# Optimization experiments

Hardware: AMD Instinct MI355X
Metric: run time of the kernel (lower is better)

## Reference

```python
import jax, jax.numpy as jnp
import numpy as np

TOPK = 0.1   # effective steady-state topk (target_topk)
TAU = 0.0    # topk_tau default: pure sparse output


def setup_inputs() -> dict:
    key = jax.random.key(0)
    x = jax.random.normal(key, (64, 256, 64, 64), dtype=jnp.float32)
    return {"x": x}


def reference(x):
    # sparse_hw: keep top-k |value| positions over the H*W axis per (n, c) row.
    n, c, h, w = x.shape
    hw = h * w
    k = int(max(1, TOPK * hw))  # 409 for 64x64 at topk=0.1
    xr = x.reshape(n, c, hw)
    # torch.topk(x_reshape.abs(), k, dim=2) -> indices of k largest magnitudes
    _, idx = jax.lax.top_k(jnp.abs(xr), k)  # idx: [n, c, k]
    # mask = zeros.scatter_(2, idx, 1)
    mask = jnp.zeros_like(xr).at[
        jnp.arange(n)[:, None, None],
        jnp.arange(c)[None, :, None],
        idx,
    ].set(1.0)
    sparse_x = (mask * xr).reshape(n, c, h, w)
    if TAU == 0.0:
        return sparse_x
    # tau blend: tau * x + (1 - tau) * sparse_x
    return TAU * x + (1.0 - TAU) * sparse_x
```

## Files before the change

kernel.cpp:

```cpp
#include <hip/hip_runtime.h>

#define HW_ 4096
#define KSEL 409
#define NCAND 256
#define LISTCAP 512

template <int N>
__device__ __forceinline__ void scan_find(const unsigned* hist, unsigned kneed,
                                          unsigned* s_bin, unsigned* s_rem, int t) {
  constexpr int C = N >> 6;
  if (t < 64) {
    const int base = N - (t + 1) * C;
    const uint4* hp = (const uint4*)(hist + base);
    unsigned sum = 0;
    #pragma unroll
    for (int j = 0; j < C / 4; ++j) {
      uint4 u = hp[j];
      sum += u.x + u.y + u.z + u.w;
    }
    unsigned inc = sum;
    #pragma unroll
    for (int off = 1; off < 64; off <<= 1) {
      unsigned u = __shfl_up(inc, off);
      if (t >= off) inc += u;
    }
    unsigned long long mb = __ballot(inc >= kneed);
    int cl = __ffsll((unsigned long long)mb) - 1;
    unsigned cumAbove = __shfl(inc, cl) - __shfl(sum, cl);
    int cbase = N - (cl + 1) * C;
    unsigned hval = (t < C) ? hist[cbase + (C - 1 - t)] : 0u;
    unsigned inc2 = hval;
    #pragma unroll
    for (int off = 1; off < 64; off <<= 1) {
      unsigned u = __shfl_up(inc2, off);
      if (t >= off) inc2 += u;
    }
    unsigned long long mb2 = __ballot(cumAbove + inc2 >= kneed);
    int cl2 = __ffsll((unsigned long long)mb2) - 1;
    if (t == cl2) {
      *s_bin = (unsigned)(cbase + (C - 1 - t));
      *s_rem = kneed - (cumAbove + inc2 - hval);
    }
  }
}

extern "C" __global__ void __launch_bounds__(256, 4)
topk_kern(const float* __restrict__ x, float* __restrict__ out) {
  __shared__ __align__(16) unsigned hist[2048];
  __shared__ unsigned sb[3];
  __shared__ unsigned cnt;
  __shared__ unsigned clist[LISTCAP];
  const int t = threadIdx.x;
  const size_t rowoff = (size_t)blockIdx.x * HW_;
  const float4* xr = (const float4*)(x + rowoff);
  float4* orow = (float4*)(out + rowoff);

  float4 v[4];
  unsigned ab[16];
  #pragma unroll
  for (int j = 0; j < 4; ++j) {
    v[j] = xr[t + j * 256];
    ab[4 * j + 0] = __float_as_uint(v[j].x) & 0x7FFFFFFFu;
    ab[4 * j + 1] = __float_as_uint(v[j].y) & 0x7FFFFFFFu;
    ab[4 * j + 2] = __float_as_uint(v[j].z) & 0x7FFFFFFFu;
    ab[4 * j + 3] = __float_as_uint(v[j].w) & 0x7FFFFFFFu;
  }

  const uint4 z4 = make_uint4(0u, 0u, 0u, 0u);
  ((uint4*)hist)[t] = z4;
  ((uint4*)hist)[t + 256] = z4;
  if (t == 0) cnt = 0;
  __syncthreads();
  #pragma unroll
  for (int i = 0; i < 16; ++i) atomicAdd(&hist[ab[i] >> 20], 1u);
  __syncthreads();
  scan_find<2048>(hist, KSEL, &sb[0], &sb[1], t);
  __syncthreads();
  const unsigned b1 = sb[0];
  const unsigned k2 = sb[1];

  #pragma unroll
  for (int i = 0; i < 16; ++i) {
    if ((ab[i] >> 20) == b1) {
      unsigned id = atomicAdd(&cnt, 1u);
      if (id < LISTCAP) clist[id] = ab[i];
    }
  }
  __syncthreads();
  const unsigned m = cnt;

  unsigned T, rem, ceq;
  if (m <= NCAND) {
    if (t < 64) {
      unsigned rq[4];
      bool vq[4];
      #pragma unroll
      for (int q = 0; q < 4; ++q) {
        unsigned idx = (unsigned)t + 64u * q;
        vq[q] = idx < m;
        rq[q] = vq[q] ? (clist[idx] & 0xFFFFFu) : 0u;
      }
      unsigned p = 0, need = k2;
      #pragma unroll
      for (int b = 19; b >= 0; --b) {
        unsigned trial = p | (1u << b);
        unsigned c = 0;
        #pragma unroll
        for (int q = 0; q < 4; ++q) {
          bool pr = vq[q] && ((rq[q] >> b) == (trial >> b));
          c += (unsigned)__popcll(__ballot(pr));
        }
        if (c >= need) p = trial;
        else need -= c;
      }
      unsigned ce = 0;
      #pragma unroll
      for (int q = 0; q < 4; ++q)
        ce += (unsigned)__popcll(__ballot(vq[q] && (rq[q] == p)));
      if (t == 0) { sb[0] = p; sb[1] = need; sb[2] = ce; }
    }
    __syncthreads();
    T = (b1 << 20) | sb[0];
    rem = sb[1];
    ceq = sb[2];
  } else {
    ((uint4*)hist)[t] = z4;
    __syncthreads();
    #pragma unroll
    for (int i = 0; i < 16; ++i)
      if ((ab[i] >> 20) == b1) atomicAdd(&hist[(ab[i] >> 10) & 0x3FFu], 1u);
    __syncthreads();
    scan_find<1024>(hist, k2, &sb[0], &sb[1], t);
    __syncthreads();
    const unsigned b2 = sb[0];
    const unsigned k3 = sb[1];
    const unsigned P = (b1 << 10) | b2;
    ((uint4*)hist)[t] = z4;
    __syncthreads();
    #pragma unroll
    for (int i = 0; i < 16; ++i)
      if ((ab[i] >> 10) == P) atomicAdd(&hist[ab[i] & 0x3FFu], 1u);
    __syncthreads();
    scan_find<1024>(hist, k3, &sb[0], &sb[1], t);
    __syncthreads();
    T = (P << 10) | sb[0];
    rem = sb[1];
    ceq = hist[sb[0]];
  }

  unsigned keepmask = 0;
  #pragma unroll
  for (int i = 0; i < 16; ++i)
    if (ab[i] > T) keepmask |= (1u << i);

  if (rem == ceq) {
    #pragma unroll
    for (int i = 0; i < 16; ++i)
      if (ab[i] == T) keepmask |= (1u << i);
  } else {
    __syncthreads();
    #pragma unroll
    for (int j = 0; j < 4; ++j) {
      unsigned c = 0;
      #pragma unroll
      for (int e = 0; e < 4; ++e)
        if (ab[4 * j + e] == T) ++c;
      hist[j * 256 + t] = c;
    }
    __syncthreads();
    if (t == 0) {
      unsigned run = 0;
      for (int i = 0; i < 1024; ++i) { unsigned h = hist[i]; hist[i] = run; run += h; }
    }
    __syncthreads();
    #pragma unroll
    for (int j = 0; j < 4; ++j) {
      unsigned r = hist[j * 256 + t];
      #pragma unroll
      for (int e = 0; e < 4; ++e) {
        if (ab[4 * j + e] == T) {
          if (r < rem) keepmask |= (1u << (4 * j + e));
          ++r;
        }
      }
    }
  }

  #pragma unroll
  for (int j = 0; j < 4; ++j) {
    float4 o;
    o.x = ((keepmask >> (4 * j + 0)) & 1u) ? v[j].x : 0.0f;
    o.y = ((keepmask >> (4 * j + 1)) & 1u) ? v[j].y : 0.0f;
    o.z = ((keepmask >> (4 * j + 2)) & 1u) ? v[j].z : 0.0f;
    o.w = ((keepmask >> (4 * j + 3)) & 1u) ? v[j].w : 0.0f;
    orow[t + j * 256] = o;
  }
}

extern "C" void kernel_launch(void* const* d_in, const int* in_sizes, int n_in,
                              void* d_out, int out_size, void* d_ws, size_t ws_size,
                              hipStream_t stream) {
  const float* x = (const float*)d_in[0];
  float* out = (float*)d_out;
  const int rows = in_sizes[0] / HW_;
  topk_kern<<<dim3(rows), dim3(256), 0, stream>>>(x, out);
}
```

Measured before the change: 433.8 us.

## Process two rows per block, prefetching second row during first row's selection

```diff
diff --git a/kernel.cpp b/kernel.cpp
--- a/kernel.cpp
+++ b/kernel.cpp
@@ -13,9 +13,12 @@
     const int base = N - (t + 1) * C;
     const uint4* hp = (const uint4*)(hist + base);
     unsigned sum = 0;
+    const int rot = t & ((C / 4) - 1);
     #pragma unroll
     for (int j = 0; j < C / 4; ++j) {
-      uint4 u = hp[j];
+      int jj = j + rot;
+      if (jj >= C / 4) jj -= C / 4;
+      uint4 u = hp[jj];
       sum += u.x + u.y + u.z + u.w;
     }
     unsigned inc = sum;
@@ -44,35 +47,17 @@
   }
 }
 
-extern "C" __global__ void __launch_bounds__(256, 4)
-topk_kern(const float* __restrict__ x, float* __restrict__ out) {
-  __shared__ __align__(16) unsigned hist[2048];
-  __shared__ unsigned sb[3];
-  __shared__ unsigned cnt;
-  __shared__ unsigned clist[LISTCAP];
-  const int t = threadIdx.x;
-  const size_t rowoff = (size_t)blockIdx.x * HW_;
-  const float4* xr = (const float4*)(x + rowoff);
-  float4* orow = (float4*)(out + rowoff);
-
-  float4 v[4];
+__device__ __forceinline__ void finish_row(const float4 (&v)[4], unsigned* hist,
+                                           unsigned* clist, unsigned* sb,
+                                           unsigned* cntp, int t, float4* orow) {
   unsigned ab[16];
   #pragma unroll
   for (int j = 0; j < 4; ++j) {
-    v[j] = xr[t + j * 256];
     ab[4 * j + 0] = __float_as_uint(v[j].x) & 0x7FFFFFFFu;
     ab[4 * j + 1] = __float_as_uint(v[j].y) & 0x7FFFFFFFu;
     ab[4 * j + 2] = __float_as_uint(v[j].z) & 0x7FFFFFFFu;
     ab[4 * j + 3] = __float_as_uint(v[j].w) & 0x7FFFFFFFu;
   }
-
-  const uint4 z4 = make_uint4(0u, 0u, 0u, 0u);
-  ((uint4*)hist)[t] = z4;
-  ((uint4*)hist)[t + 256] = z4;
-  if (t == 0) cnt = 0;
-  __syncthreads();
-  #pragma unroll
-  for (int i = 0; i < 16; ++i) atomicAdd(&hist[ab[i] >> 20], 1u);
   __syncthreads();
   scan_find<2048>(hist, KSEL, &sb[0], &sb[1], t);
   __syncthreads();
@@ -82,12 +67,12 @@
   #pragma unroll
   for (int i = 0; i < 16; ++i) {
     if ((ab[i] >> 20) == b1) {
-      unsigned id = atomicAdd(&cnt, 1u);
+      unsigned id = atomicAdd(cntp, 1u);
       if (id < LISTCAP) clist[id] = ab[i];
     }
   }
   __syncthreads();
-  const unsigned m = cnt;
+  const unsigned m = *cntp;
 
   unsigned T, rem, ceq;
   if (m <= NCAND) {
@@ -124,6 +109,8 @@
     rem = sb[1];
     ceq = sb[2];
   } else {
+    const uint4 z4 = make_uint4(0u, 0u, 0u, 0u);
+    __syncthreads();
     ((uint4*)hist)[t] = z4;
     __syncthreads();
     #pragma unroll
@@ -135,6 +122,7 @@
     const unsigned b2 = sb[0];
     const unsigned k3 = sb[1];
     const unsigned P = (b1 << 10) | b2;
+    __syncthreads();
     ((uint4*)hist)[t] = z4;
     __syncthreads();
     #pragma unroll
@@ -197,11 +185,64 @@
   }
 }
 
+extern "C" __global__ void __launch_bounds__(256, 4)
+topk_kern(const float* __restrict__ x, float* __restrict__ out) {
+  __shared__ __align__(16) unsigned hist[2048];
+  __shared__ unsigned sb[3];
+  __shared__ unsigned cnt;
+  __shared__ unsigned clist[LISTCAP];
+  const int t = threadIdx.x;
+  const size_t rowoffA = (size_t)blockIdx.x * (2 * HW_);
+  const float4* xrA = (const float4*)(x + rowoffA);
+  const float4* xrB = xrA + (HW_ / 4);
+  float4* orowA = (float4*)(out + rowoffA);
+  float4* orowB = orowA + (HW_ / 4);
+
+  float4 vA[4], vB[4];
+  #pragma unroll
+  for (int j = 0; j < 4; ++j) vA[j] = xrA[t + j * 256];
+
+  const uint4 z4 = make_uint4(0u, 0u, 0u, 0u);
+  ((uint4*)hist)[t] = z4;
+  ((uint4*)hist)[t + 256] = z4;
+  if (t == 0) cnt = 0;
+  __syncthreads();
+
+  #pragma unroll
+  for (int j = 0; j < 4; ++j) {
+    atomicAdd(&hist[(__float_as_uint(vA[j].x) & 0x7FFFFFFFu) >> 20], 1u);
+    atomicAdd(&hist[(__float_as_uint(vA[j].y) & 0x7FFFFFFFu) >> 20], 1u);
+    atomicAdd(&hist[(__float_as_uint(vA[j].z) & 0x7FFFFFFFu) >> 20], 1u);
+    atomicAdd(&hist[(__float_as_uint(vA[j].w) & 0x7FFFFFFFu) >> 20], 1u);
+  }
+
+  #pragma unroll
+  for (int j = 0; j < 4; ++j) vB[j] = xrB[t + j * 256];
+
+  finish_row(vA, hist, clist, sb, &cnt, t, orowA);
+
+  __syncthreads();
+  ((uint4*)hist)[t] = z4;
+  ((uint4*)hist)[t + 256] = z4;
+  if (t == 0) cnt = 0;
+  __syncthreads();
+
+  #pragma unroll
+  for (int j = 0; j < 4; ++j) {
+    atomicAdd(&hist[(__float_as_uint(vB[j].x) & 0x7FFFFFFFu) >> 20], 1u);
+    atomicAdd(&hist[(__float_as_uint(vB[j].y) & 0x7FFFFFFFu) >> 20], 1u);
+    atomicAdd(&hist[(__float_as_uint(vB[j].z) & 0x7FFFFFFFu) >> 20], 1u);
+    atomicAdd(&hist[(__float_as_uint(vB[j].w) & 0x7FFFFFFFu) >> 20], 1u);
+  }
+
+  finish_row(vB, hist, clist, sb, &cnt, t, orowB);
+}
+
 extern "C" void kernel_launch(void* const* d_in, const int* in_sizes, int n_in,
                               void* d_out, int out_size, void* d_ws, size_t ws_size,
                               hipStream_t stream) {
   const float* x = (const float*)d_in[0];
   float* out = (float*)d_out;
   const int rows = in_sizes[0] / HW_;
-  topk_kern<<<dim3(rows), dim3(256), 0, stream>>>(x, out);
-}
+  topk_kern<<<dim3(rows / 2), dim3(256), 0, stream>>>(x, out);
+}
```

Result: slower. 446.6 us (+2.9%).
